# Kernel tuning notes

Hardware: AMD Instinct MI355X
Metric: run time of the kernel (lower is better)

## Reference

```python
import jax, jax.numpy as jnp
import numpy as np

N = 2708
IN_C = 1433
OUT_C = 64


def setup_inputs() -> dict:
    key = jax.random.key(0)
    k1, k2, k3, k4, k5, k6, k7 = jax.random.split(key, 7)
    X = jax.random.normal(k1, (N, IN_C), dtype=jnp.float32)
    A = jax.random.randint(k2, (N, N), 0, 2, dtype=jnp.int32)  # dense binary adjacency mask
    # Graph Fourier basis: orthonormal-ish random matrix (QR of gaussian)
    U = jnp.linalg.qr(jax.random.normal(k3, (N, N), dtype=jnp.float32))[0]
    s = 1.0 / np.sqrt(IN_C)
    W_K = jax.random.normal(k4, (OUT_C, IN_C), dtype=jnp.float32) * s
    W_Q = jax.random.normal(k5, (OUT_C, IN_C), dtype=jnp.float32) * s
    W_V = jax.random.normal(k6, (OUT_C, IN_C), dtype=jnp.float32) * s
    lmbd = jax.random.uniform(k7, (N, 1), dtype=jnp.float32)
    return {"X": X, "A": A, "U": U, "W_K": W_K, "W_Q": W_Q, "W_V": W_V, "lmbd": lmbd}


def reference(X, A, U, W_K, W_Q, W_V, lmbd):
    # Linear projections (torch nn.Linear: x @ W.T)
    K = X @ W_K.T  # [N, d]
    Q = X @ W_Q.T  # [N, d]
    V = X @ W_V.T  # [N, d]
    d_k = K.shape[-1]
    E = (Q @ K.T) / d_k  # [N, N]
    # spectral filtering: igft(lmbd * gft(E)) = U @ (lmbd * (U^T @ E))
    E = jnp.abs(U @ (lmbd * (U.T @ E)))
    # masked softmax over neighbors; dropout p=0 in eval mode (no-op)
    E_masked = jnp.where(A == 0, -jnp.inf, E)
    alpha = jax.nn.softmax(E_masked, axis=-1)
    H = alpha @ V  # [N, d]
    return H
```

## Files before the change

kernel.cpp:

```cpp
#include <hip/hip_runtime.h>

#define NV 2708
#define INC 1433
#define XCOLS 1472
#define UDIM 2752
#define PSTR 2720
#define BSTR 2752
#define SLAB ((size_t)(2752*64))
#define MWPR 88
#define NSP 8
#define NSU 22

typedef __attribute__((ext_vector_type(8))) short bf16x8;
typedef __attribute__((ext_vector_type(4))) float f32x4;
typedef __attribute__((ext_vector_type(4))) unsigned short u16x4;

__device__ __forceinline__ unsigned short f2bf(float f){
  union { float f; unsigned int i; } v; v.f = f;
  return (unsigned short)((v.i + 0x7fffu + ((v.i >> 16) & 1u)) >> 16);
}

__global__ __launch_bounds__(256) void convert_all(
    const float* __restrict__ X, const float* __restrict__ WK,
    const float* __restrict__ WQ, const float* __restrict__ WV,
    const float* __restrict__ U, const int* __restrict__ A,
    unsigned short* __restrict__ Xbf, unsigned short* __restrict__ Wbf,
    unsigned short* __restrict__ Ubf, unsigned int* __restrict__ Abits)
{
  const int bx = blockIdx.x;
  const int tid = threadIdx.x;
  if (bx < 2752){
    const int row = bx;
    unsigned short* dst = Ubf + (size_t)row*UDIM;
    if (row < NV){
      const float* src = U + (size_t)row*NV;
      for (int c4 = tid; c4 < 688; c4 += 256){
        float4 v = make_float4(0.f,0.f,0.f,0.f);
        if (c4 < 677) v = *(const float4*)(src + c4*4);
        u16x4 h = { f2bf(v.x), f2bf(v.y), f2bf(v.z), f2bf(v.w) };
        *(u16x4*)(dst + c4*4) = h;
      }
    } else {
      u16x4 zz = {0,0,0,0};
      for (int c4 = tid; c4 < 688; c4 += 256) *(u16x4*)(dst + c4*4) = zz;
    }
  } else if (bx < 5504){
    const int row = bx - 2752;
    unsigned short* dst = Xbf + (size_t)row*XCOLS;
    if (row < NV){
      const float* src = X + (size_t)row*INC;
      for (int c = tid; c < XCOLS; c += 256)
        dst[c] = (c < INC) ? f2bf(src[c]) : (unsigned short)0;
    } else {
      for (int c = tid; c < XCOLS; c += 256) dst[c] = 0;
    }
  } else if (bx < 5696){
    const int row = bx - 5504;
    const float* s = (row < 64) ? WK : (row < 128) ? WQ : WV;
    const float* src = s + (size_t)(row & 63)*INC;
    unsigned short* dst = Wbf + (size_t)row*XCOLS;
    for (int c = tid; c < XCOLS; c += 256)
      dst[c] = (c < INC) ? f2bf(src[c]) : (unsigned short)0;
  } else {
    const int i = bx - 5696;
    const int lane = tid & 63, wave = tid >> 6;
    const int* arow = A + (size_t)i*NV;
    unsigned int* drow = Abits + (size_t)i*MWPR;
    if (tid < 2) drow[86 + tid] = 0u;
    for (int g = wave; g < 43; g += 4){
      int j = g*64 + lane;
      int a = (j < NV) ? arow[j] : 0;
      unsigned long long m = __ballot(a != 0);
      if (lane == 0){
        drow[2*g]     = (unsigned int)m;
        drow[2*g + 1] = (unsigned int)(m >> 32);
      }
    }
  }
}

__global__ __launch_bounds__(256) void proj(
    const unsigned short* __restrict__ Xbf, const unsigned short* __restrict__ Wbf,
    float* __restrict__ part)
{
  __shared__ __align__(16) unsigned short At[64*72];
  __shared__ __align__(16) unsigned short Bt[64*72];
  const int tid = threadIdx.x;
  const int lane = tid & 63, wave = tid >> 6, quad = lane >> 4, lr = lane & 15;
  const int m0 = blockIdx.x * 64;
  const int s  = blockIdx.y, z = blockIdx.z;
  const int kbeg = s * 192, kend = min(kbeg + 192, XCOLS);
  const int wm = (wave & 1) * 32, wn = (wave >> 1) * 32;
  const unsigned short* Wz = Wbf + (size_t)z*64*XCOLS;
  const int srow = wave*8 + (lane >> 3), seg = lane & 7;
  f32x4 acc[2][2] = {};

  for (int k0 = kbeg; k0 < kend; k0 += 64){
    #pragma unroll
    for (int e = 0; e < 2; e++){
      int row = e*32 + srow;
      bf16x8 xa = *(const bf16x8*)(Xbf + (size_t)(m0+row)*XCOLS + k0 + seg*8);
      bf16x8 wb = *(const bf16x8*)(Wz  + (size_t)row*XCOLS      + k0 + seg*8);
      *(bf16x8*)&At[row*72 + seg*8] = xa;
      *(bf16x8*)&Bt[row*72 + seg*8] = wb;
    }
    __syncthreads();
    #pragma unroll
    for (int ks = 0; ks < 2; ks++){
      bf16x8 af[2], bv[2];
      #pragma unroll
      for (int t = 0; t < 2; t++){
        af[t] = *(const bf16x8*)&At[(wm + t*16 + lr)*72 + ks*32 + quad*8];
        bv[t] = *(const bf16x8*)&Bt[(wn + t*16 + lr)*72 + ks*32 + quad*8];
      }
      #pragma unroll
      for (int tm = 0; tm < 2; tm++)
        #pragma unroll
        for (int tn = 0; tn < 2; tn++)
          acc[tm][tn] = __builtin_amdgcn_mfma_f32_16x16x32_bf16(af[tm], bv[tn], acc[tm][tn], 0, 0, 0);
    }
    __syncthreads();
  }
  float* dst = part + (size_t)(z*NSP + s) * SLAB;
  #pragma unroll
  for (int tm = 0; tm < 2; tm++)
    #pragma unroll
    for (int tn = 0; tn < 2; tn++)
      #pragma unroll
      for (int e = 0; e < 4; e++)
        dst[(size_t)(m0 + wm + tm*16 + quad*4 + e)*64 + wn + tn*16 + lr] = acc[tm][tn][e];
}

__global__ __launch_bounds__(256) void reduce_proj(
    const float* __restrict__ part, unsigned short* __restrict__ K16f,
    unsigned short* __restrict__ QT16, unsigned short* __restrict__ VTf)
{
  int idx = blockIdx.x*256 + threadIdx.x;
  int z = blockIdx.y;
  int m = idx >> 6, c = idx & 63;
  const float* base = part + (size_t)z*NSP*SLAB + idx;
  float v = 0.f;
  #pragma unroll
  for (int s = 0; s < NSP; s++) v += base[s*SLAB];
  unsigned short h = (m < NV) ? f2bf(v) : (unsigned short)0;
  if (z == 0){
    if (m < 2720) K16f[((m>>4)*2 + (c>>5))*512 + (m&15)*32 + (c&31)] = h;
  } else if (z == 1){
    QT16[(size_t)c*BSTR + m] = h;
  } else {
    if (m < 2720) VTf[(m>>5)*2048 + c*32 + (m&31)] = h;
  }
}

__global__ __launch_bounds__(256) void gemmG(
    const unsigned short* __restrict__ Ubf, const unsigned short* __restrict__ QT,
    float* __restrict__ part)
{
  __shared__ __align__(16) unsigned short At[64*72];
  __shared__ __align__(16) unsigned short Bt[64*72];
  const int tid = threadIdx.x;
  const int lane = tid & 63, wave = tid >> 6, quad = lane >> 4, lr = lane & 15;
  const int m0 = blockIdx.x * 64;
  const int s  = blockIdx.y;
  const int kbeg = s * 128, kend = min(kbeg + 128, UDIM);
  const int wm = (wave & 1) * 32, wn = (wave >> 1) * 32;
  const int bc = tid >> 2, bseg = tid & 3;
  const int ml = (lane & 15)*4, koff = wave*16 + (lane >> 4);
  f32x4 acc[2][2] = {};

  for (int k0 = kbeg; k0 < kend; k0 += 64){
    #pragma unroll
    for (int e = 0; e < 4; e++){
      int kl = koff + e*4;
      u16x4 v = *(const u16x4*)(Ubf + (size_t)(k0+kl)*UDIM + m0 + ml);
      At[(ml+0)*72 + kl] = v[0];
      At[(ml+1)*72 + kl] = v[1];
      At[(ml+2)*72 + kl] = v[2];
      At[(ml+3)*72 + kl] = v[3];
    }
    {
      const unsigned short* q = QT + (size_t)bc*BSTR + k0 + bseg*16;
      *(bf16x8*)&Bt[bc*72 + bseg*16]     = *(const bf16x8*)(q);
      *(bf16x8*)&Bt[bc*72 + bseg*16 + 8] = *(const bf16x8*)(q + 8);
    }
    __syncthreads();
    #pragma unroll
    for (int ks = 0; ks < 2; ks++){
      bf16x8 af[2], bv[2];
      #pragma unroll
      for (int t = 0; t < 2; t++){
        af[t] = *(const bf16x8*)&At[(wm + t*16 + lr)*72 + ks*32 + quad*8];
        bv[t] = *(const bf16x8*)&Bt[(wn + t*16 + lr)*72 + ks*32 + quad*8];
      }
      #pragma unroll
      for (int tm = 0; tm < 2; tm++)
        #pragma unroll
        for (int tn = 0; tn < 2; tn++)
          acc[tm][tn] = __builtin_amdgcn_mfma_f32_16x16x32_bf16(af[tm], bv[tn], acc[tm][tn], 0, 0, 0);
    }
    __syncthreads();
  }
  float* dst = part + (size_t)s * SLAB;
  #pragma unroll
  for (int tm = 0; tm < 2; tm++)
    #pragma unroll
    for (int tn = 0; tn < 2; tn++)
      #pragma unroll
      for (int e = 0; e < 4; e++)
        dst[(size_t)(m0 + wm + tm*16 + quad*4 + e)*64 + wn + tn*16 + lr] = acc[tm][tn][e];
}

__global__ __launch_bounds__(256) void reduce_g(
    const float* __restrict__ part, const float* __restrict__ lm,
    unsigned short* __restrict__ G2T)
{
  int idx = blockIdx.x*256 + threadIdx.x;
  int m = idx >> 6, c = idx & 63;
  const float* base = part + idx;
  float v = 0.f;
  #pragma unroll
  for (int s = 0; s < NSU; s++) v += base[s*SLAB];
  unsigned short h = 0;
  if (m < NV) h = f2bf(v * lm[m] * (1.0f/64.0f));
  G2T[(size_t)c*BSTR + m] = h;
}

__global__ __launch_bounds__(256) void gemmF(
    const unsigned short* __restrict__ Ubf, const unsigned short* __restrict__ G2T,
    float* __restrict__ part)
{
  __shared__ __align__(16) unsigned short At[64*72];
  __shared__ __align__(16) unsigned short Bt[64*72];
  const int tid = threadIdx.x;
  const int lane = tid & 63, wave = tid >> 6, quad = lane >> 4, lr = lane & 15;
  const int m0 = blockIdx.x * 64;
  const int s  = blockIdx.y;
  const int kbeg = s * 128, kend = min(kbeg + 128, UDIM);
  const int wm = (wave & 1) * 32, wn = (wave >> 1) * 32;
  const int bc = tid >> 2, bseg = tid & 3;
  const int srow = wave*8 + (lane >> 3), seg = lane & 7;
  f32x4 acc[2][2] = {};

  for (int k0 = kbeg; k0 < kend; k0 += 64){
    #pragma unroll
    for (int e = 0; e < 2; e++){
      int row = e*32 + srow;
      bf16x8 ua = *(const bf16x8*)(Ubf + (size_t)(m0+row)*UDIM + k0 + seg*8);
      *(bf16x8*)&At[row*72 + seg*8] = ua;
    }
    {
      const unsigned short* g = G2T + (size_t)bc*BSTR + k0 + bseg*16;
      *(bf16x8*)&Bt[bc*72 + bseg*16]     = *(const bf16x8*)(g);
      *(bf16x8*)&Bt[bc*72 + bseg*16 + 8] = *(const bf16x8*)(g + 8);
    }
    __syncthreads();
    #pragma unroll
    for (int ks = 0; ks < 2; ks++){
      bf16x8 af[2], bv[2];
      #pragma unroll
      for (int t = 0; t < 2; t++){
        af[t] = *(const bf16x8*)&At[(wm + t*16 + lr)*72 + ks*32 + quad*8];
        bv[t] = *(const bf16x8*)&Bt[(wn + t*16 + lr)*72 + ks*32 + quad*8];
      }
      #pragma unroll
      for (int tm = 0; tm < 2; tm++)
        #pragma unroll
        for (int tn = 0; tn < 2; tn++)
          acc[tm][tn] = __builtin_amdgcn_mfma_f32_16x16x32_bf16(af[tm], bv[tn], acc[tm][tn], 0, 0, 0);
    }
    __syncthreads();
  }
  float* dst = part + (size_t)s * SLAB;
  #pragma unroll
  for (int tm = 0; tm < 2; tm++)
    #pragma unroll
    for (int tn = 0; tn < 2; tn++)
      #pragma unroll
      for (int e = 0; e < 4; e++)
        dst[(size_t)(m0 + wm + tm*16 + quad*4 + e)*64 + wn + tn*16 + lr] = acc[tm][tn][e];
}

__global__ __launch_bounds__(256) void fused_attn(
    const float* __restrict__ partF, const unsigned short* __restrict__ K16f,
    const unsigned int* __restrict__ Abits, const unsigned short* __restrict__ VTf,
    float* __restrict__ Hout)
{
  __shared__ __align__(16) unsigned short pbuf[8*PSTR];
  __shared__ __align__(16) unsigned short fbuf[8*64];
  __shared__ unsigned int mrow[8*MWPR];
  __shared__ float swave[4][8];
  __shared__ float rinv[8];
  const int tid  = threadIdx.x;
  const int lane = tid & 63, wave = tid >> 6;
  const int quad = lane >> 4, lr = lane & 15;
  const int i0 = blockIdx.x * 8;

  #pragma unroll
  for (int h = 0; h < 2; h++){
    int idx = h*256 + tid;
    const float* base = partF + (size_t)(i0 + (idx >> 6))*64 + (idx & 63);
    float v = 0.f;
    #pragma unroll
    for (int s = 0; s < NSU; s++) v += base[s*SLAB];
    fbuf[idx] = f2bf(v);
  }
  for (int idx = tid; idx < 8*MWPR; idx += 256){
    int r = idx / MWPR;
    unsigned int v = 0;
    if (i0 + r < NV) v = Abits[(size_t)(i0 + r)*MWPR + (idx - r*MWPR)];
    mrow[idx] = v;
  }
  __syncthreads();

  const bf16x8 af0 = *(const bf16x8*)&fbuf[(lr & 7)*64 + quad*8];
  const bf16x8 af1 = *(const bf16x8*)&fbuf[(lr & 7)*64 + 32 + quad*8];
  float psum[4] = {0.f, 0.f, 0.f, 0.f};
  {
    int t = wave;
    const unsigned short* kb = K16f + t*1024 + lr*32 + quad*8;
    bf16x8 b0 = *(const bf16x8*)(kb);
    bf16x8 b1 = *(const bf16x8*)(kb + 512);
    while (t < 170){
      int tn = t + 4;
      bf16x8 n0 = b0, n1 = b1;
      if (tn < 170){
        const unsigned short* nb = K16f + tn*1024 + lr*32 + quad*8;
        n0 = *(const bf16x8*)(nb);
        n1 = *(const bf16x8*)(nb + 512);
      }
      f32x4 sv = {};
      sv = __builtin_amdgcn_mfma_f32_16x16x32_bf16(af0, b0, sv, 0, 0, 0);
      sv = __builtin_amdgcn_mfma_f32_16x16x32_bf16(af1, b1, sv, 0, 0, 0);
      if (quad < 2){
        int col = t*16 + lr;
        int wsh = col >> 5, bit = col & 31;
        #pragma unroll
        for (int e = 0; e < 4; e++){
          int r = quad*4 + e;
          float p = 0.f;
          if ((mrow[r*MWPR + wsh] >> bit) & 1u) p = __expf(fabsf(sv[e]));
          psum[e] += p;
          pbuf[r*PSTR + col] = f2bf(p);
        }
      }
      b0 = n0; b1 = n1; t = tn;
    }
  }
  #pragma unroll
  for (int e = 0; e < 4; e++){
    float v = psum[e];
    #pragma unroll
    for (int o = 1; o <= 8; o <<= 1) v += __shfl_xor(v, o, 64);
    if (lr == 0 && quad < 2) swave[wave][quad*4 + e] = v;
  }
  __syncthreads();
  if (tid < 8){
    float sum = swave[0][tid] + swave[1][tid] + swave[2][tid] + swave[3][tid];
    rinv[tid] = (sum > 0.f) ? (1.f/sum) : 0.f;
  }
  __syncthreads();

  const int c0 = wave * 16;
  const int mr = lr & 7;
  f32x4 acc = {};
  {
    bf16x8 bv = *(const bf16x8*)&VTf[(c0 + lr)*32 + quad*8];
    for (int kt = 0; kt < 85; kt++){
      bf16x8 bn = bv;
      if (kt + 1 < 85) bn = *(const bf16x8*)&VTf[(kt+1)*2048 + (c0 + lr)*32 + quad*8];
      bf16x8 af = *(const bf16x8*)&pbuf[mr*PSTR + kt*32 + quad*8];
      acc = __builtin_amdgcn_mfma_f32_16x16x32_bf16(af, bv, acc, 0, 0, 0);
      bv = bn;
    }
  }
  if (quad < 2){
    #pragma unroll
    for (int e = 0; e < 4; e++){
      int r = quad*4 + e;
      int i = i0 + r;
      if (i < NV) Hout[(size_t)i*64 + c0 + lr] = acc[e] * rinv[r];
    }
  }
}

extern "C" void kernel_launch(void* const* d_in, const int* in_sizes, int n_in,
                              void* d_out, int out_size, void* d_ws, size_t ws_size,
                              hipStream_t stream){
  (void)in_sizes; (void)n_in; (void)out_size; (void)ws_size;
  const float* X  = (const float*)d_in[0];
  const int*   A  = (const int*)d_in[1];
  const float* U  = (const float*)d_in[2];
  const float* WK = (const float*)d_in[3];
  const float* WQ = (const float*)d_in[4];
  const float* WV = (const float*)d_in[5];
  const float* lm = (const float*)d_in[6];

  char* ws = (char*)d_ws;
  size_t off = 0;
  auto alloc = [&](size_t bytes){ size_t o = off; off = (off + bytes + 255) & ~(size_t)255; return o; };
  float*          part = (float*)(ws + alloc(24*SLAB*4));
  unsigned short* Ubf  = (unsigned short*)(ws + alloc((size_t)UDIM*UDIM*2));
  unsigned short* Xbf  = (unsigned short*)(ws + alloc((size_t)UDIM*XCOLS*2));
  unsigned short* Wbf  = (unsigned short*)(ws + alloc((size_t)192*XCOLS*2));
  unsigned short* K16f = (unsigned short*)(ws + alloc((size_t)170*1024*2));
  unsigned short* QT16 = (unsigned short*)(ws + alloc((size_t)64*BSTR*2));
  unsigned short* G2T  = (unsigned short*)(ws + alloc((size_t)64*BSTR*2));
  unsigned short* VTf  = (unsigned short*)(ws + alloc((size_t)85*2048*2));
  unsigned int*   Abits= (unsigned int*)(ws + alloc((size_t)NV*MWPR*4));

  convert_all<<<dim3(8404), 256, 0, stream>>>(X, WK, WQ, WV, U, A, Xbf, Wbf, Ubf, Abits);
  proj<<<dim3(43, NSP, 3), 256, 0, stream>>>(Xbf, Wbf, part);
  reduce_proj<<<dim3(688, 3), 256, 0, stream>>>(part, K16f, QT16, VTf);
  gemmG<<<dim3(43, NSU), 256, 0, stream>>>(Ubf, QT16, part);
  reduce_g<<<dim3(688), 256, 0, stream>>>(part, lm, G2T);
  gemmF<<<dim3(43, NSU), 256, 0, stream>>>(Ubf, G2T, part);
  fused_attn<<<dim3((NV + 7)/8), 256, 0, stream>>>(part, K16f, Abits, VTf, (float*)d_out);
}
```

Before: 196.7 us.

## Halve split-K slabs, widen convert blocks, restructure attention to 4 rows per 512-thread block

Halves the split-K factor for the projection and both spectral GEMMs, so each block covers twice the K range and fewer partial slabs need writing and summing. convert_all moves to 512-thread blocks. fused_attn now handles 4 rows per block with 8 waves: score tiles are split across 8 waves, and the P·V reduction is split across two K halves and combined through shared memory. The aim is more blocks and less wasted MFMA lane work in attention, plus less partial-sum traffic, at the cost of fewer parallel blocks in the GEMMs.

```diff
diff --git a/kernel.cpp b/kernel.cpp
--- a/kernel.cpp
+++ b/kernel.cpp
@@ -8,8 +8,8 @@
 #define BSTR 2752
 #define SLAB ((size_t)(2752*64))
 #define MWPR 88
-#define NSP 8
-#define NSU 22
+#define NSP 4
+#define NSU 11
 
 typedef __attribute__((ext_vector_type(8))) short bf16x8;
 typedef __attribute__((ext_vector_type(4))) float f32x4;
@@ -20,7 +20,7 @@
   return (unsigned short)((v.i + 0x7fffu + ((v.i >> 16) & 1u)) >> 16);
 }
 
-__global__ __launch_bounds__(256) void convert_all(
+__global__ __launch_bounds__(512) void convert_all(
     const float* __restrict__ X, const float* __restrict__ WK,
     const float* __restrict__ WQ, const float* __restrict__ WV,
     const float* __restrict__ U, const int* __restrict__ A,
@@ -34,7 +34,7 @@
     unsigned short* dst = Ubf + (size_t)row*UDIM;
     if (row < NV){
       const float* src = U + (size_t)row*NV;
-      for (int c4 = tid; c4 < 688; c4 += 256){
+      for (int c4 = tid; c4 < 688; c4 += 512){
         float4 v = make_float4(0.f,0.f,0.f,0.f);
         if (c4 < 677) v = *(const float4*)(src + c4*4);
         u16x4 h = { f2bf(v.x), f2bf(v.y), f2bf(v.z), f2bf(v.w) };
@@ -42,24 +42,24 @@
       }
     } else {
       u16x4 zz = {0,0,0,0};
-      for (int c4 = tid; c4 < 688; c4 += 256) *(u16x4*)(dst + c4*4) = zz;
+      for (int c4 = tid; c4 < 688; c4 += 512) *(u16x4*)(dst + c4*4) = zz;
     }
   } else if (bx < 5504){
     const int row = bx - 2752;
     unsigned short* dst = Xbf + (size_t)row*XCOLS;
     if (row < NV){
       const float* src = X + (size_t)row*INC;
-      for (int c = tid; c < XCOLS; c += 256)
+      for (int c = tid; c < XCOLS; c += 512)
         dst[c] = (c < INC) ? f2bf(src[c]) : (unsigned short)0;
     } else {
-      for (int c = tid; c < XCOLS; c += 256) dst[c] = 0;
+      for (int c = tid; c < XCOLS; c += 512) dst[c] = 0;
     }
   } else if (bx < 5696){
     const int row = bx - 5504;
     const float* s = (row < 64) ? WK : (row < 128) ? WQ : WV;
     const float* src = s + (size_t)(row & 63)*INC;
     unsigned short* dst = Wbf + (size_t)row*XCOLS;
-    for (int c = tid; c < XCOLS; c += 256)
+    for (int c = tid; c < XCOLS; c += 512)
       dst[c] = (c < INC) ? f2bf(src[c]) : (unsigned short)0;
   } else {
     const int i = bx - 5696;
@@ -67,7 +67,7 @@
     const int* arow = A + (size_t)i*NV;
     unsigned int* drow = Abits + (size_t)i*MWPR;
     if (tid < 2) drow[86 + tid] = 0u;
-    for (int g = wave; g < 43; g += 4){
+    for (int g = wave; g < 43; g += 8){
       int j = g*64 + lane;
       int a = (j < NV) ? arow[j] : 0;
       unsigned long long m = __ballot(a != 0);
@@ -89,7 +89,7 @@
   const int lane = tid & 63, wave = tid >> 6, quad = lane >> 4, lr = lane & 15;
   const int m0 = blockIdx.x * 64;
   const int s  = blockIdx.y, z = blockIdx.z;
-  const int kbeg = s * 192, kend = min(kbeg + 192, XCOLS);
+  const int kbeg = s * 384, kend = min(kbeg + 384, XCOLS);
   const int wm = (wave & 1) * 32, wn = (wave >> 1) * 32;
   const unsigned short* Wz = Wbf + (size_t)z*64*XCOLS;
   const int srow = wave*8 + (lane >> 3), seg = lane & 7;
@@ -162,7 +162,7 @@
   const int lane = tid & 63, wave = tid >> 6, quad = lane >> 4, lr = lane & 15;
   const int m0 = blockIdx.x * 64;
   const int s  = blockIdx.y;
-  const int kbeg = s * 128, kend = min(kbeg + 128, UDIM);
+  const int kbeg = s * 256, kend = min(kbeg + 256, UDIM);
   const int wm = (wave & 1) * 32, wn = (wave >> 1) * 32;
   const int bc = tid >> 2, bseg = tid & 3;
   const int ml = (lane & 15)*4, koff = wave*16 + (lane >> 4);
@@ -235,7 +235,7 @@
   const int lane = tid & 63, wave = tid >> 6, quad = lane >> 4, lr = lane & 15;
   const int m0 = blockIdx.x * 64;
   const int s  = blockIdx.y;
-  const int kbeg = s * 128, kend = min(kbeg + 128, UDIM);
+  const int kbeg = s * 256, kend = min(kbeg + 256, UDIM);
   const int wm = (wave & 1) * 32, wn = (wave >> 1) * 32;
   const int bc = tid >> 2, bseg = tid & 3;
   const int srow = wave*8 + (lane >> 3), seg = lane & 7;
@@ -280,40 +280,37 @@
         dst[(size_t)(m0 + wm + tm*16 + quad*4 + e)*64 + wn + tn*16 + lr] = acc[tm][tn][e];
 }
 
-__global__ __launch_bounds__(256) void fused_attn(
+__global__ __launch_bounds__(512) void fused_attn(
     const float* __restrict__ partF, const unsigned short* __restrict__ K16f,
     const unsigned int* __restrict__ Abits, const unsigned short* __restrict__ VTf,
     float* __restrict__ Hout)
 {
-  __shared__ __align__(16) unsigned short pbuf[8*PSTR];
-  __shared__ __align__(16) unsigned short fbuf[8*64];
-  __shared__ unsigned int mrow[8*MWPR];
-  __shared__ float swave[4][8];
-  __shared__ float rinv[8];
+  __shared__ __align__(16) unsigned short pbuf[4*PSTR];
+  __shared__ __align__(16) unsigned short fbuf[4*64];
+  __shared__ unsigned int mrow[4*MWPR];
+  __shared__ float swave[8][4];
+  __shared__ float rinv[4];
+  __shared__ float cacc[2][4][16][4];
   const int tid  = threadIdx.x;
   const int lane = tid & 63, wave = tid >> 6;
   const int quad = lane >> 4, lr = lane & 15;
-  const int i0 = blockIdx.x * 8;
-
-  #pragma unroll
-  for (int h = 0; h < 2; h++){
-    int idx = h*256 + tid;
-    const float* base = partF + (size_t)(i0 + (idx >> 6))*64 + (idx & 63);
+  const int i0 = blockIdx.x * 4;
+
+  if (tid < 256){
+    const float* base = partF + (size_t)(i0 + (tid >> 6))*64 + (tid & 63);
     float v = 0.f;
     #pragma unroll
     for (int s = 0; s < NSU; s++) v += base[s*SLAB];
-    fbuf[idx] = f2bf(v);
-  }
-  for (int idx = tid; idx < 8*MWPR; idx += 256){
+    fbuf[tid] = f2bf(v);
+  }
+  for (int idx = tid; idx < 4*MWPR; idx += 512){
     int r = idx / MWPR;
-    unsigned int v = 0;
-    if (i0 + r < NV) v = Abits[(size_t)(i0 + r)*MWPR + (idx - r*MWPR)];
-    mrow[idx] = v;
+    mrow[idx] = Abits[(size_t)(i0 + r)*MWPR + (idx - r*MWPR)];
   }
   __syncthreads();
 
-  const bf16x8 af0 = *(const bf16x8*)&fbuf[(lr & 7)*64 + quad*8];
-  const bf16x8 af1 = *(const bf16x8*)&fbuf[(lr & 7)*64 + 32 + quad*8];
+  const bf16x8 af0 = *(const bf16x8*)&fbuf[(lr & 3)*64 + quad*8];
+  const bf16x8 af1 = *(const bf16x8*)&fbuf[(lr & 3)*64 + 32 + quad*8];
   float psum[4] = {0.f, 0.f, 0.f, 0.f};
   {
     int t = wave;
@@ -321,7 +318,7 @@
     bf16x8 b0 = *(const bf16x8*)(kb);
     bf16x8 b1 = *(const bf16x8*)(kb + 512);
     while (t < 170){
-      int tn = t + 4;
+      int tn = t + 8;
       bf16x8 n0 = b0, n1 = b1;
       if (tn < 170){
         const unsigned short* nb = K16f + tn*1024 + lr*32 + quad*8;
@@ -331,16 +328,15 @@
       f32x4 sv = {};
       sv = __builtin_amdgcn_mfma_f32_16x16x32_bf16(af0, b0, sv, 0, 0, 0);
       sv = __builtin_amdgcn_mfma_f32_16x16x32_bf16(af1, b1, sv, 0, 0, 0);
-      if (quad < 2){
+      if (quad == 0){
         int col = t*16 + lr;
         int wsh = col >> 5, bit = col & 31;
         #pragma unroll
         for (int e = 0; e < 4; e++){
-          int r = quad*4 + e;
           float p = 0.f;
-          if ((mrow[r*MWPR + wsh] >> bit) & 1u) p = __expf(fabsf(sv[e]));
+          if ((mrow[e*MWPR + wsh] >> bit) & 1u) p = __expf(fabsf(sv[e]));
           psum[e] += p;
-          pbuf[r*PSTR + col] = f2bf(p);
+          pbuf[e*PSTR + col] = f2bf(p);
         }
       }
       b0 = n0; b1 = n1; t = tn;
@@ -351,35 +347,39 @@
     float v = psum[e];
     #pragma unroll
     for (int o = 1; o <= 8; o <<= 1) v += __shfl_xor(v, o, 64);
-    if (lr == 0 && quad < 2) swave[wave][quad*4 + e] = v;
+    if (quad == 0 && lr == 0) swave[wave][e] = v;
   }
   __syncthreads();
-  if (tid < 8){
-    float sum = swave[0][tid] + swave[1][tid] + swave[2][tid] + swave[3][tid];
-    rinv[tid] = (sum > 0.f) ? (1.f/sum) : 0.f;
+  if (tid < 4){
+    float s = 0.f;
+    #pragma unroll
+    for (int w = 0; w < 8; w++) s += swave[w][tid];
+    rinv[tid] = (s > 0.f) ? (1.f/s) : 0.f;
   }
   __syncthreads();
 
-  const int c0 = wave * 16;
-  const int mr = lr & 7;
+  const int kh = wave >> 2, cg = wave & 3;
+  const int kbegc = kh ? 43 : 0, kendc = kh ? 85 : 43;
   f32x4 acc = {};
   {
-    bf16x8 bv = *(const bf16x8*)&VTf[(c0 + lr)*32 + quad*8];
-    for (int kt = 0; kt < 85; kt++){
+    bf16x8 bv = *(const bf16x8*)&VTf[kbegc*2048 + (cg*16 + lr)*32 + quad*8];
+    for (int kt = kbegc; kt < kendc; kt++){
       bf16x8 bn = bv;
-      if (kt + 1 < 85) bn = *(const bf16x8*)&VTf[(kt+1)*2048 + (c0 + lr)*32 + quad*8];
-      bf16x8 af = *(const bf16x8*)&pbuf[mr*PSTR + kt*32 + quad*8];
+      if (kt + 1 < kendc) bn = *(const bf16x8*)&VTf[(kt+1)*2048 + (cg*16 + lr)*32 + quad*8];
+      bf16x8 af = *(const bf16x8*)&pbuf[(lr & 3)*PSTR + kt*32 + quad*8];
       acc = __builtin_amdgcn_mfma_f32_16x16x32_bf16(af, bv, acc, 0, 0, 0);
       bv = bn;
     }
   }
-  if (quad < 2){
-    #pragma unroll
-    for (int e = 0; e < 4; e++){
-      int r = quad*4 + e;
-      int i = i0 + r;
-      if (i < NV) Hout[(size_t)i*64 + c0 + lr] = acc[e] * rinv[r];
-    }
+  if (quad == 0){
+    #pragma unroll
+    for (int e = 0; e < 4; e++) cacc[kh][cg][lr][e] = acc[e];
+  }
+  __syncthreads();
+  if (tid < 256){
+    int e = tid >> 6, c = tid & 63;
+    float v = (cacc[0][c>>4][c&15][e] + cacc[1][c>>4][c&15][e]) * rinv[e];
+    Hout[(size_t)(i0 + e)*64 + c] = v;
   }
 }
 
@@ -398,7 +398,7 @@
   char* ws = (char*)d_ws;
   size_t off = 0;
   auto alloc = [&](size_t bytes){ size_t o = off; off = (off + bytes + 255) & ~(size_t)255; return o; };
-  float*          part = (float*)(ws + alloc(24*SLAB*4));
+  float*          part = (float*)(ws + alloc(12*SLAB*4));
   unsigned short* Ubf  = (unsigned short*)(ws + alloc((size_t)UDIM*UDIM*2));
   unsigned short* Xbf  = (unsigned short*)(ws + alloc((size_t)UDIM*XCOLS*2));
   unsigned short* Wbf  = (unsigned short*)(ws + alloc((size_t)192*XCOLS*2));
@@ -408,11 +408,11 @@
   unsigned short* VTf  = (unsigned short*)(ws + alloc((size_t)85*2048*2));
   unsigned int*   Abits= (unsigned int*)(ws + alloc((size_t)NV*MWPR*4));
 
-  convert_all<<<dim3(8404), 256, 0, stream>>>(X, WK, WQ, WV, U, A, Xbf, Wbf, Ubf, Abits);
+  convert_all<<<dim3(8404), 512, 0, stream>>>(X, WK, WQ, WV, U, A, Xbf, Wbf, Ubf, Abits);
   proj<<<dim3(43, NSP, 3), 256, 0, stream>>>(Xbf, Wbf, part);
   reduce_proj<<<dim3(688, 3), 256, 0, stream>>>(part, K16f, QT16, VTf);
   gemmG<<<dim3(43, NSU), 256, 0, stream>>>(Ubf, QT16, part);
   reduce_g<<<dim3(688), 256, 0, stream>>>(part, lm, G2T);
   gemmF<<<dim3(43, NSU), 256, 0, stream>>>(Ubf, G2T, part);
-  fused_attn<<<dim3((NV + 7)/8), 256, 0, stream>>>(part, K16f, Abits, VTf, (float*)d_out);
-}
+  fused_attn<<<dim3(NV/4), 512, 0, stream>>>(part, K16f, Abits, VTf, (float*)d_out);
+}
```

Measured after the change: 197.1 us. About the same (+0.2%).
